# Kernel optimization log

Measured on AMD Instinct MI355X. Metric: run time of the kernel, lower is better.

The kernel has to match this reference:

```python
import jax, jax.numpy as jnp
import numpy as np

N = 100000       # num_nodes
E = 1200000      # num_edges
D = 64           # input feature dim
K = 10           # propagation iterations
ALPHA = 0.1      # teleport probability
H0, H1 = 64, 32  # units_list


def setup_inputs() -> dict:
    key = jax.random.key(0)
    ks = jax.random.split(key, 5)
    x = jax.random.normal(ks[0], (N, D), dtype=jnp.float32)
    edge_index = jax.random.randint(ks[1], (2, E), 0, N, dtype=jnp.int32)
    edge_weight = jax.random.uniform(ks[2], (E,), dtype=jnp.float32)
    # glorot-ish dense params per units_list=[64, 32]
    W0 = jax.random.normal(ks[3], (D, H0), dtype=jnp.float32) * (1.0 / np.sqrt(D))
    b0 = jnp.zeros((H0,), jnp.float32)
    W1 = jax.random.normal(ks[4], (H0, H1), dtype=jnp.float32) * (1.0 / np.sqrt(H0))
    b1 = jnp.zeros((H1,), jnp.float32)
    return dict(x=x, edge_index=edge_index, edge_weight=edge_weight,
                W0=W0, b0=b0, W1=W1, b1=b1)


def reference(x, edge_index, edge_weight, W0, b0, W1, b1):
    n = x.shape[0]
    loop = jnp.arange(n, dtype=edge_index.dtype)
    # GCN renorm: add self-loops with fill weight 1, symmetric D^-1/2 A D^-1/2
    row = jnp.concatenate([edge_index[0], loop])
    col = jnp.concatenate([edge_index[1], loop])
    w = jnp.concatenate([edge_weight, jnp.ones((n,), x.dtype)])
    deg = jax.ops.segment_sum(w, row, num_segments=n)
    dinv = jax.lax.rsqrt(jnp.maximum(deg, 1e-12))
    nw = dinv[row] * w * dinv[col]          # [E+N] normalized edge weights

    # k-hop propagation with running sum: (1/K) sum_k A_hat^k x
    h = x
    acc = jnp.zeros_like(x)
    for _ in range(K):
        h = jax.ops.segment_sum(nw[:, None] * h[row], col, num_segments=n)
        acc = acc + h
    out = acc * ((1.0 - ALPHA) / K) + ALPHA * x

    # dense MLP stack: all but last activated with relu, last linear
    out = jax.nn.relu(out @ W0 + b0)
    out = out @ W1 + b1
    return out
```

## Files before the change

### kernel.cpp

```cpp
#include <hip/hip_runtime.h>
#include <hip/hip_bf16.h>

#define NTHREADS 256
#define GB 1024
#define NB 256
#define BW 512

typedef unsigned int uint32;
typedef unsigned long long u64;


__device__ __forceinline__ float blo(uint32 u) { return __uint_as_float(u << 16); }
__device__ __forceinline__ float bhi(uint32 u) { return __uint_as_float(u & 0xffff0000u); }

__device__ __forceinline__ unsigned short bf16bits(float f) {
    __hip_bfloat16 h = __float2bfloat16(f);
    return *reinterpret_cast<unsigned short*>(&h);
}
__device__ __forceinline__ uint32 pk2(float a, float b) {
    return (uint32)bf16bits(a) | ((uint32)bf16bits(b) << 16);
}


__global__ void deginit_k(float* deg, int n) {
    int i = blockIdx.x * blockDim.x + threadIdx.x;
    if (i < n) deg[i] = 0.f;
}


__global__ __launch_bounds__(256) void histdeg_k(const int* __restrict__ row,
                                                 const int* __restrict__ col,
                                                 const float* __restrict__ w,
                                                 float* deg, int* __restrict__ bh,
                                                 int e, int ch) {
    __shared__ int hist[NB];
    int tid = threadIdx.x;
    hist[tid] = 0;
    __syncthreads();
    int beg = blockIdx.x * ch;
    int end = min(e, beg + ch);
    for (int i = beg + tid; i < end; i += 256) {
        unsafeAtomicAdd(&deg[row[i]], w[i]);
        atomicAdd(&hist[col[i] >> 9], 1);
    }
    __syncthreads();
    bh[(size_t)tid * GB + blockIdx.x] = hist[tid];
}


__global__ __launch_bounds__(256) void scanb_k(int* bh, int* tb) {
    __shared__ int s[256];
    int b = blockIdx.x;
    int tid = threadIdx.x;
    size_t base = (size_t)b * GB + tid * 4;
    int v0 = bh[base], v1 = bh[base + 1], v2 = bh[base + 2], v3 = bh[base + 3];
    int tsum = v0 + v1 + v2 + v3;
    s[tid] = tsum;
    __syncthreads();
    for (int off = 1; off < 256; off <<= 1) {
        int t = (tid >= off) ? s[tid - off] : 0;
        __syncthreads();
        s[tid] += t;
        __syncthreads();
    }
    int excl = s[tid] - tsum;
    bh[base] = excl;
    bh[base + 1] = excl + v0;
    bh[base + 2] = excl + v0 + v1;
    bh[base + 3] = excl + v0 + v1 + v2;
    if (tid == 255) tb[b] = s[255];
}


__global__ void scant_k(const int* __restrict__ tb, int* gb) {
    __shared__ int s[256];
    int tid = threadIdx.x;
    int v = tb[tid];
    s[tid] = v;
    __syncthreads();
    for (int off = 1; off < 256; off <<= 1) {
        int t = (tid >= off) ? s[tid - off] : 0;
        __syncthreads();
        s[tid] += t;
        __syncthreads();
    }
    gb[tid] = s[tid] - v;
    if (tid == 255) gb[256] = s[255];
}


__global__ __launch_bounds__(256) void bscatter_k(const int* __restrict__ row,
                                                  const int* __restrict__ col,
                                                  const float* __restrict__ w,
                                                  const int* __restrict__ bh,
                                                  const int* __restrict__ gb,
                                                  int* __restrict__ st_col,
                                                  u64* __restrict__ st_rw,
                                                  int e, int ch) {
    __shared__ int hist[NB];
    int tid = threadIdx.x;
    hist[tid] = 0;
    __syncthreads();
    int beg = blockIdx.x * ch;
    int end = min(e, beg + ch);
    for (int i = beg + tid; i < end; i += 256) {
        int c = col[i];
        int bk = c >> 9;
        int rank = atomicAdd(&hist[bk], 1);
        int slot = gb[bk] + bh[(size_t)bk * GB + blockIdx.x] + rank;
        st_col[slot] = c;
        st_rw[slot] = (u64)(uint32)row[i] | ((u64)__float_as_uint(w[i]) << 32);
    }
}


__global__ __launch_bounds__(256) void bcount_k(const int* __restrict__ st_col,
                                                const int* __restrict__ gb,
                                                int* __restrict__ counts, int n) {
    __shared__ int cnt[BW];
    int bk = blockIdx.x;
    int tid = threadIdx.x;
    cnt[tid] = 0; cnt[tid + 256] = 0;
    __syncthreads();
    int beg = gb[bk], end = gb[bk + 1];
    for (int j = beg + tid; j < end; j += 256)
        atomicAdd(&cnt[st_col[j] & (BW - 1)], 1);
    __syncthreads();
    int n0 = bk * BW + tid, n1 = n0 + 256;
    if (n0 < n) counts[n0] = cnt[tid];
    if (n1 < n) counts[n1] = cnt[tid + 256];
}


__global__ void scan1_k(const int* __restrict__ counts, int* offsets, int* blockSums, int n) {
    __shared__ int s[256];
    int tid = threadIdx.x;
    int idx = blockIdx.x * 256 + tid;
    int v = (idx < n) ? counts[idx] : 0;
    s[tid] = v;
    __syncthreads();
    for (int off = 1; off < 256; off <<= 1) {
        int t = (tid >= off) ? s[tid - off] : 0;
        __syncthreads();
        s[tid] += t;
        __syncthreads();
    }
    if (idx < n) offsets[idx] = s[tid] - v;
    if (tid == 255) blockSums[blockIdx.x] = s[255];
}

__global__ void scan2_k(int* blockSums, int nb) {
    __shared__ int s[1024];
    int tid = threadIdx.x;
    int v = (tid < nb) ? blockSums[tid] : 0;
    s[tid] = v;
    __syncthreads();
    for (int off = 1; off < 1024; off <<= 1) {
        int t = (tid >= off) ? s[tid - off] : 0;
        __syncthreads();
        s[tid] += t;
        __syncthreads();
    }
    if (tid < nb) blockSums[tid] = s[tid] - v;
}

__global__ void scan3_k(int* offsets, const int* __restrict__ blockSums, int n, int total) {
    int idx = blockIdx.x * blockDim.x + threadIdx.x;
    if (idx < n) offsets[idx] += blockSums[idx >> 8];
    if (idx == n) offsets[n] = total;
}


__global__ __launch_bounds__(256) void bplace_k(const int* __restrict__ st_col,
                                                const u64* __restrict__ st_rw,
                                                const int* __restrict__ gb,
                                                const int* __restrict__ offsets,
                                                u64* __restrict__ csr) {
    __shared__ int cnt[BW];
    int bk = blockIdx.x;
    int tid = threadIdx.x;
    cnt[tid] = 0; cnt[tid + 256] = 0;
    __syncthreads();
    int beg = gb[bk], end = gb[bk + 1];
    for (int j = beg + tid; j < end; j += 256) {
        int c = st_col[j];
        int rank = atomicAdd(&cnt[c & (BW - 1)], 1);
        csr[offsets[c] + rank] = st_rw[j];
    }
}


__global__ void dinv_k(const float* __restrict__ deg, float* dinv, int n) {
    int i = blockIdx.x * blockDim.x + threadIdx.x;
    if (i < n) dinv[i] = rsqrtf(fmaxf(deg[i] + 1.0f, 1e-12f));
}


__global__ void uxseed_k(const float* __restrict__ x, const float* __restrict__ dinv,
                         uint32* __restrict__ ux, int pairs) {
    int i = blockIdx.x * blockDim.x + threadIdx.x;
    if (i < pairs) {
        float di = dinv[i >> 5];
        float2 v = ((const float2*)x)[i];
        ux[i] = pk2(di * v.x, di * v.y);
    }
}


template <int MODE>
__global__ __launch_bounds__(256) void horner4n_k(
    const unsigned short* __restrict__ u_in,
    unsigned short* __restrict__ u_out,
    unsigned short* __restrict__ ybf,
    const unsigned short* __restrict__ ux_bf,
    const float* __restrict__ x,
    const float* __restrict__ dinv,
    const int* __restrict__ offsets,
    const u64* __restrict__ csr,
    int n)
{
    int wv = __builtin_amdgcn_readfirstlane(threadIdx.x >> 6);
    int lane = threadIdx.x & 63;
    int g = lane >> 3;
    int s = lane & 7;
    int nbase = blockIdx.x * 16 + wv * 4;

    int bb[4], ee[4];
#pragma unroll
    for (int m = 0; m < 4; ++m) {
        int node = nbase + m;
        if (node < n) { bb[m] = offsets[node]; ee[m] = offsets[node + 1]; }
        else          { bb[m] = 0; ee[m] = 0; }
    }
    int maxd = max(max(ee[0] - bb[0], ee[1] - bb[1]), max(ee[2] - bb[2], ee[3] - bb[3]));

    float acc[4][8];
#pragma unroll
    for (int m = 0; m < 4; ++m)
#pragma unroll
        for (int i = 0; i < 8; ++i) acc[m][i] = 0.f;

    u64 sw[4];
#pragma unroll
    for (int m = 0; m < 4; ++m) {
        int j = bb[m] + g;
        sw[m] = (j < ee[m]) ? csr[j] : 0ull;
    }

    for (int off = 0; off < maxd; off += 8) {
        uint4 q[4];
#pragma unroll
        for (int m = 0; m < 4; ++m)
            q[m] = ((const uint4*)(u_in + (size_t)(uint32)(sw[m] & 0xffffffffu) * 64))[s];
        u64 swn[4];
#pragma unroll
        for (int m = 0; m < 4; ++m) {
            int j = bb[m] + off + 8 + g;
            swn[m] = (j < ee[m]) ? csr[j] : 0ull;
        }
#pragma unroll
        for (int m = 0; m < 4; ++m) {
            float w = __uint_as_float((uint32)(sw[m] >> 32));
            acc[m][0] = fmaf(w, blo(q[m].x), acc[m][0]);
            acc[m][1] = fmaf(w, bhi(q[m].x), acc[m][1]);
            acc[m][2] = fmaf(w, blo(q[m].y), acc[m][2]);
            acc[m][3] = fmaf(w, bhi(q[m].y), acc[m][3]);
            acc[m][4] = fmaf(w, blo(q[m].z), acc[m][4]);
            acc[m][5] = fmaf(w, bhi(q[m].z), acc[m][5]);
            acc[m][6] = fmaf(w, blo(q[m].w), acc[m][6]);
            acc[m][7] = fmaf(w, bhi(q[m].w), acc[m][7]);
        }
#pragma unroll
        for (int m = 0; m < 4; ++m) sw[m] = swn[m];
    }

#pragma unroll
    for (int mask = 8; mask <= 32; mask <<= 1)
#pragma unroll
        for (int m = 0; m < 4; ++m)
#pragma unroll
            for (int i = 0; i < 8; ++i)
                acc[m][i] += __shfl_xor(acc[m][i], mask);

    float t[8];
#pragma unroll
    for (int i = 0; i < 8; ++i) {
        float a01 = (g == 0) ? acc[0][i] : acc[1][i];
        float a23 = (g == 2) ? acc[2][i] : acc[3][i];
        t[i] = (g < 2) ? a01 : a23;
    }

    if (g < 4) {
        int node = nbase + g;
        if (node < n) {
            float di = dinv[node];
            uint4 zq = ((const uint4*)(u_in + (size_t)node * 64))[s];
            t[0] += blo(zq.x); t[1] += bhi(zq.x);
            t[2] += blo(zq.y); t[3] += bhi(zq.y);
            t[4] += blo(zq.z); t[5] += bhi(zq.z);
            t[6] += blo(zq.w); t[7] += bhi(zq.w);
            if (MODE == 0) {
                float dd = di * di;
                uint4 xq = ((const uint4*)(ux_bf + (size_t)node * 64))[s];
                uint4 o;
                o.x = pk2(fmaf(dd, t[0], blo(xq.x)), fmaf(dd, t[1], bhi(xq.x)));
                o.y = pk2(fmaf(dd, t[2], blo(xq.y)), fmaf(dd, t[3], bhi(xq.y)));
                o.z = pk2(fmaf(dd, t[4], blo(xq.z)), fmaf(dd, t[5], bhi(xq.z)));
                o.w = pk2(fmaf(dd, t[6], blo(xq.w)), fmaf(dd, t[7], bhi(xq.w)));
                ((uint4*)(u_out + (size_t)node * 64))[s] = o;
            } else {
                float c = 0.09f * di;
                const float4* xr = (const float4*)(x + (size_t)node * 64);
                float4 xa = xr[s * 2], xb = xr[s * 2 + 1];
                uint4 o;
                o.x = pk2(fmaf(c, t[0], 0.1f * xa.x), fmaf(c, t[1], 0.1f * xa.y));
                o.y = pk2(fmaf(c, t[2], 0.1f * xa.z), fmaf(c, t[3], 0.1f * xa.w));
                o.z = pk2(fmaf(c, t[4], 0.1f * xb.x), fmaf(c, t[5], 0.1f * xb.y));
                o.w = pk2(fmaf(c, t[6], 0.1f * xb.z), fmaf(c, t[7], 0.1f * xb.w));
                ((uint4*)(ybf + (size_t)node * 64))[s] = o;
            }
        }
    }
}


__global__ __launch_bounds__(256) void mlp_k(const unsigned short* __restrict__ ybf,
                                             const float* __restrict__ W0,
                                             const float* __restrict__ b0,
                                             const float* __restrict__ W1,
                                             const float* __restrict__ b1,
                                             float* __restrict__ out, int n) {
    __shared__ float W0s[64 * 64];
    __shared__ float W1s[64 * 32];
    __shared__ float b0s[64];
    __shared__ float b1s[32];
    __shared__ float z[32][64];
    __shared__ float hid[32][64];
    int tid = threadIdx.x;
    for (int i = tid; i < 64 * 64; i += 256) W0s[i] = W0[i];
    for (int i = tid; i < 64 * 32; i += 256) W1s[i] = W1[i];
    if (tid < 64) b0s[tid] = b0[tid];
    else if (tid < 96) b1s[tid - 64] = b1[tid - 64];

    int base = blockIdx.x * 32;
    const uint32* y32 = (const uint32*)ybf;
    for (int r = 0; r < 4; ++r) {
        int idx = r * 256 + tid;
        int nn = idx >> 5, f2 = idx & 31;
        int node = base + nn;
        uint32 v = (node < n) ? y32[(size_t)node * 32 + f2] : 0u;
        z[nn][f2 * 2]     = blo(v);
        z[nn][f2 * 2 + 1] = bhi(v);
    }
    __syncthreads();
    for (int r = 0; r < 8; ++r) {
        int idx = r * 256 + tid;
        int nn = idx >> 6, j = idx & 63;
        float s = b0s[j];
#pragma unroll
        for (int i = 0; i < 64; ++i) s += z[nn][i] * W0s[i * 64 + j];
        hid[nn][j] = fmaxf(s, 0.f);
    }
    __syncthreads();
    for (int r = 0; r < 4; ++r) {
        int idx = r * 256 + tid;
        int nn = idx >> 5, o = idx & 31;
        int node = base + nn;
        if (node >= n) continue;
        float s = b1s[o];
#pragma unroll
        for (int i = 0; i < 64; ++i) s += hid[nn][i] * W1s[i * 32 + o];
        out[(size_t)node * 32 + o] = s;
    }
}


extern "C" void kernel_launch(void* const* d_in, const int* in_sizes, int n_in,
                              void* d_out, int out_size, void* d_ws, size_t ws_size,
                              hipStream_t stream) {
    const float* x   = (const float*)d_in[0];
    const int*   ei  = (const int*)d_in[1];
    const float* ew  = (const float*)d_in[2];
    const float* W0  = (const float*)d_in[3];
    const float* b0  = (const float*)d_in[4];
    const float* W1  = (const float*)d_in[5];
    const float* b1  = (const float*)d_in[6];
    float* out = (float*)d_out;

    const int N = in_sizes[0] / 64;
    const int E = in_sizes[2];
    const int* row = ei;
    const int* col = ei + E;

    char* p = (char*)d_ws;
    auto alloc = [&](size_t bytes) -> void* {
        void* r = (void*)p;
        p += (bytes + 255) & ~(size_t)255;
        return r;
    };
    float* deg       = (float*)alloc((size_t)N * 4);
    float* dinv      = (float*)alloc((size_t)N * 4);
    int*   bh        = (int*)alloc((size_t)NB * GB * 4);
    int*   tb        = (int*)alloc(NB * 4);
    int*   gb        = (int*)alloc((NB + 1) * 4);
    int*   st_col    = (int*)alloc((size_t)E * 4);
    u64*   st_rw     = (u64*)alloc((size_t)E * 8);
    int*   counts    = (int*)alloc((size_t)N * 4);
    int*   offsets   = (int*)alloc((size_t)(N + 1) * 4);
    int    nb        = (N + 255) / 256;
    int*   blockSums = (int*)alloc((size_t)nb * 4);
    u64*   csr       = (u64*)alloc((size_t)E * 8);
    unsigned short* uxbf = (unsigned short*)alloc((size_t)N * 64 * 2);
    unsigned short* uA   = (unsigned short*)alloc((size_t)N * 64 * 2);
    unsigned short* uB   = (unsigned short*)alloc((size_t)N * 64 * 2);
    unsigned short* ybf  = (unsigned short*)alloc((size_t)N * 64 * 2);

    int gN = (N + NTHREADS - 1) / NTHREADS;
    int ch = (E + GB - 1) / GB;

    deginit_k<<<gN, NTHREADS, 0, stream>>>(deg, N);
    histdeg_k<<<GB, 256, 0, stream>>>(row, col, ew, deg, bh, E, ch);
    scanb_k<<<NB, 256, 0, stream>>>(bh, tb);
    scant_k<<<1, 256, 0, stream>>>(tb, gb);
    bscatter_k<<<GB, 256, 0, stream>>>(row, col, ew, bh, gb, st_col, st_rw, E, ch);
    bcount_k<<<NB, 256, 0, stream>>>(st_col, gb, counts, N);

    scan1_k<<<nb, 256, 0, stream>>>(counts, offsets, blockSums, N);
    scan2_k<<<1, 1024, 0, stream>>>(blockSums, nb);
    scan3_k<<<(N + 1 + NTHREADS - 1) / NTHREADS, NTHREADS, 0, stream>>>(offsets, blockSums, N, E);
    bplace_k<<<NB, 256, 0, stream>>>(st_col, st_rw, gb, offsets, csr);

    dinv_k<<<gN, NTHREADS, 0, stream>>>(deg, dinv, N);
    int pairs = N * 32;
    uxseed_k<<<(pairs + NTHREADS - 1) / NTHREADS, NTHREADS, 0, stream>>>(x, dinv,
                                                                         (uint32*)uxbf, pairs);

    int gP = (N + 15) / 16;
    const unsigned short* ui = uxbf;
    for (int k = 1; k <= 9; ++k) {
        unsigned short* uo = (ui == uA) ? uB : uA;
        horner4n_k<0><<<gP, 256, 0, stream>>>(ui, uo, nullptr, uxbf, x, dinv, offsets, csr, N);
        ui = uo;
    }
    horner4n_k<1><<<gP, 256, 0, stream>>>(ui, nullptr, ybf, uxbf, x, dinv, offsets, csr, N);

    mlp_k<<<(N + 31) / 32, 256, 0, stream>>>(ybf, W0, b0, W1, b1, out, N);
}
```

Before: 508.2 us.

## Compute degrees via row-bucketed sort and run MLP on MFMA bf16

Two separate changes. First, global float atomics on the degree array are replaced by a second bucket sort keyed by row: rows are histogrammed and scattered into the csr buffer, which is reused as scratch, and a per-bucket kernel accumulates degrees in shared memory and writes dinv directly. This removes contended global atomics and the deginit and dinv kernels, at the cost of an extra 8-byte scatter pass over all edges. Second, the MLP uses bf16 MFMA 16x16x32 instructions with swizzled transposed weights in LDS instead of scalar FP32 loops, which lowers precision of the hidden layer and weights to bf16.

After: 428.9 us. 15.6% less time.

```diff
diff --git a/kernel.cpp b/kernel.cpp
--- a/kernel.cpp
+++ b/kernel.cpp
@@ -8,6 +8,8 @@
 
 typedef unsigned int uint32;
 typedef unsigned long long u64;
+typedef __bf16 bf16x8 __attribute__((ext_vector_type(8)));
+typedef float f32x4 __attribute__((ext_vector_type(4)));
 
 
 __device__ __forceinline__ float blo(uint32 u) { return __uint_as_float(u << 16); }
@@ -22,29 +24,23 @@
 }
 
 
-__global__ void deginit_k(float* deg, int n) {
-    int i = blockIdx.x * blockDim.x + threadIdx.x;
-    if (i < n) deg[i] = 0.f;
-}
-
-
-__global__ __launch_bounds__(256) void histdeg_k(const int* __restrict__ row,
-                                                 const int* __restrict__ col,
-                                                 const float* __restrict__ w,
-                                                 float* deg, int* __restrict__ bh,
-                                                 int e, int ch) {
-    __shared__ int hist[NB];
-    int tid = threadIdx.x;
-    hist[tid] = 0;
+__global__ __launch_bounds__(256) void histcols_k(const int* __restrict__ row,
+                                                  const int* __restrict__ col,
+                                                  int* __restrict__ bh, int* __restrict__ bh2,
+                                                  int e, int ch) {
+    __shared__ int h1[NB], h2[NB];
+    int tid = threadIdx.x;
+    h1[tid] = 0; h2[tid] = 0;
     __syncthreads();
     int beg = blockIdx.x * ch;
     int end = min(e, beg + ch);
     for (int i = beg + tid; i < end; i += 256) {
-        unsafeAtomicAdd(&deg[row[i]], w[i]);
-        atomicAdd(&hist[col[i] >> 9], 1);
-    }
-    __syncthreads();
-    bh[(size_t)tid * GB + blockIdx.x] = hist[tid];
+        atomicAdd(&h1[col[i] >> 9], 1);
+        atomicAdd(&h2[row[i] >> 9], 1);
+    }
+    __syncthreads();
+    bh[(size_t)tid * GB + blockIdx.x] = h1[tid];
+    bh2[(size_t)tid * GB + blockIdx.x] = h2[tid];
 }
 
 
@@ -72,7 +68,7 @@
 }
 
 
-__global__ void scant_k(const int* __restrict__ tb, int* gb) {
+__global__ void scant_k(const int* __restrict__ tb, int* gbase) {
     __shared__ int s[256];
     int tid = threadIdx.x;
     int v = tb[tid];
@@ -84,8 +80,8 @@
         s[tid] += t;
         __syncthreads();
     }
-    gb[tid] = s[tid] - v;
-    if (tid == 255) gb[256] = s[255];
+    gbase[tid] = s[tid] - v;
+    if (tid == 255) gbase[256] = s[255];
 }
 
 
@@ -93,24 +89,55 @@
                                                   const int* __restrict__ col,
                                                   const float* __restrict__ w,
                                                   const int* __restrict__ bh,
+                                                  const int* __restrict__ bh2,
                                                   const int* __restrict__ gb,
+                                                  const int* __restrict__ gb2,
                                                   int* __restrict__ st_col,
                                                   u64* __restrict__ st_rw,
+                                                  u64* __restrict__ st2,
                                                   int e, int ch) {
-    __shared__ int hist[NB];
-    int tid = threadIdx.x;
-    hist[tid] = 0;
+    __shared__ int h1[NB], h2[NB];
+    int tid = threadIdx.x;
+    h1[tid] = 0; h2[tid] = 0;
     __syncthreads();
     int beg = blockIdx.x * ch;
     int end = min(e, beg + ch);
     for (int i = beg + tid; i < end; i += 256) {
-        int c = col[i];
+        int c = col[i], r = row[i];
+        float wv = w[i];
+        u64 rec = (u64)(uint32)r | ((u64)__float_as_uint(wv) << 32);
         int bk = c >> 9;
-        int rank = atomicAdd(&hist[bk], 1);
+        int rank = atomicAdd(&h1[bk], 1);
         int slot = gb[bk] + bh[(size_t)bk * GB + blockIdx.x] + rank;
         st_col[slot] = c;
-        st_rw[slot] = (u64)(uint32)row[i] | ((u64)__float_as_uint(w[i]) << 32);
-    }
+        st_rw[slot] = rec;
+        int bk2 = r >> 9;
+        int rank2 = atomicAdd(&h2[bk2], 1);
+        int slot2 = gb2[bk2] + bh2[(size_t)bk2 * GB + blockIdx.x] + rank2;
+        st2[slot2] = rec;
+    }
+}
+
+
+__global__ __launch_bounds__(256) void bdeg_k(const u64* __restrict__ st2,
+                                              const int* __restrict__ gb2,
+                                              float* __restrict__ dinv, int n) {
+    __shared__ float facc[BW];
+    int bk = blockIdx.x;
+    int tid = threadIdx.x;
+    facc[tid] = 0.f; facc[tid + 256] = 0.f;
+    __syncthreads();
+    int beg = gb2[bk], end = gb2[bk + 1];
+    for (int j = beg + tid; j < end; j += 256) {
+        u64 v = st2[j];
+        int r = (int)(uint32)v;
+        float wv = __uint_as_float((uint32)(v >> 32));
+        atomicAdd(&facc[r & (BW - 1)], wv);
+    }
+    __syncthreads();
+    int n0 = bk * BW + tid, n1 = n0 + 256;
+    if (n0 < n) dinv[n0] = rsqrtf(fmaxf(facc[tid] + 1.f, 1e-12f));
+    if (n1 < n) dinv[n1] = rsqrtf(fmaxf(facc[tid + 256] + 1.f, 1e-12f));
 }
 
 
@@ -187,12 +214,6 @@
         int rank = atomicAdd(&cnt[c & (BW - 1)], 1);
         csr[offsets[c] + rank] = st_rw[j];
     }
-}
-
-
-__global__ void dinv_k(const float* __restrict__ deg, float* dinv, int n) {
-    int i = blockIdx.x * blockDim.x + threadIdx.x;
-    if (i < n) dinv[i] = rsqrtf(fmaxf(deg[i] + 1.0f, 1e-12f));
 }
 
 
@@ -324,53 +345,76 @@
 }
 
 
-__global__ __launch_bounds__(256) void mlp_k(const unsigned short* __restrict__ ybf,
-                                             const float* __restrict__ W0,
-                                             const float* __restrict__ b0,
-                                             const float* __restrict__ W1,
-                                             const float* __restrict__ b1,
-                                             float* __restrict__ out, int n) {
-    __shared__ float W0s[64 * 64];
-    __shared__ float W1s[64 * 32];
-    __shared__ float b0s[64];
-    __shared__ float b1s[32];
-    __shared__ float z[32][64];
-    __shared__ float hid[32][64];
-    int tid = threadIdx.x;
-    for (int i = tid; i < 64 * 64; i += 256) W0s[i] = W0[i];
-    for (int i = tid; i < 64 * 32; i += 256) W1s[i] = W1[i];
+__global__ __launch_bounds__(256) void mlp_mfma_k(const unsigned short* __restrict__ ybf,
+                                                  const float* __restrict__ W0,
+                                                  const float* __restrict__ b0,
+                                                  const float* __restrict__ W1,
+                                                  const float* __restrict__ b1,
+                                                  float* __restrict__ out, int n) {
+    __shared__ __align__(16) unsigned short W0t[64 * 64];
+    __shared__ __align__(16) unsigned short W1t[32 * 64];
+    __shared__ __align__(16) unsigned short hidL[4][16 * 64];
+    __shared__ float b0s[64], b1s[32];
+    int tid = threadIdx.x;
+    for (int i = tid; i < 64 * 64; i += 256) {
+        int k = i >> 6, j = i & 63;
+        W0t[j * 64 + (k ^ ((j & 7) << 3))] = bf16bits(W0[i]);
+    }
+    for (int i = tid; i < 64 * 32; i += 256) {
+        int k = i >> 5, j = i & 31;
+        W1t[j * 64 + (k ^ ((j & 7) << 3))] = bf16bits(W1[i]);
+    }
     if (tid < 64) b0s[tid] = b0[tid];
     else if (tid < 96) b1s[tid - 64] = b1[tid - 64];
-
-    int base = blockIdx.x * 32;
-    const uint32* y32 = (const uint32*)ybf;
-    for (int r = 0; r < 4; ++r) {
-        int idx = r * 256 + tid;
-        int nn = idx >> 5, f2 = idx & 31;
-        int node = base + nn;
-        uint32 v = (node < n) ? y32[(size_t)node * 32 + f2] : 0u;
-        z[nn][f2 * 2]     = blo(v);
-        z[nn][f2 * 2 + 1] = bhi(v);
-    }
-    __syncthreads();
-    for (int r = 0; r < 8; ++r) {
-        int idx = r * 256 + tid;
-        int nn = idx >> 6, j = idx & 63;
-        float s = b0s[j];
-#pragma unroll
-        for (int i = 0; i < 64; ++i) s += z[nn][i] * W0s[i * 64 + j];
-        hid[nn][j] = fmaxf(s, 0.f);
-    }
-    __syncthreads();
-    for (int r = 0; r < 4; ++r) {
-        int idx = r * 256 + tid;
-        int nn = idx >> 5, o = idx & 31;
-        int node = base + nn;
-        if (node >= n) continue;
-        float s = b1s[o];
-#pragma unroll
-        for (int i = 0; i < 64; ++i) s += hid[nn][i] * W1s[i * 32 + o];
-        out[(size_t)node * 32 + o] = s;
+    __syncthreads();
+
+    int wave = tid >> 6, lane = tid & 63;
+    int r = lane & 15, g = lane >> 4;
+    int nbase = blockIdx.x * 64 + wave * 16;
+
+    int nodeA = min(nbase + r, n - 1);
+    const bf16x8* yrow = (const bf16x8*)(ybf + (size_t)nodeA * 64);
+    bf16x8 A0 = yrow[g];
+    bf16x8 A1 = yrow[4 + g];
+
+#pragma unroll
+    for (int t = 0; t < 4; ++t) {
+        int j = t * 16 + r;
+        int sj = j & 7;
+        const bf16x8* wcol = (const bf16x8*)(W0t + j * 64);
+        bf16x8 B0 = wcol[g ^ sj];
+        bf16x8 B1 = wcol[(4 + g) ^ sj];
+        float bv = b0s[j];
+        f32x4 acc = {bv, bv, bv, bv};
+        acc = __builtin_amdgcn_mfma_f32_16x16x32_bf16(A0, B0, acc, 0, 0, 0);
+        acc = __builtin_amdgcn_mfma_f32_16x16x32_bf16(A1, B1, acc, 0, 0, 0);
+#pragma unroll
+        for (int v = 0; v < 4; ++v) {
+            int i = g * 4 + v;
+            hidL[wave][i * 64 + (j ^ ((i & 7) << 3))] = bf16bits(fmaxf(acc[v], 0.f));
+        }
+    }
+
+    const bf16x8* hrow = (const bf16x8*)(hidL[wave] + r * 64);
+    int sr = r & 7;
+    bf16x8 HA0 = hrow[g ^ sr];
+    bf16x8 HA1 = hrow[(4 + g) ^ sr];
+#pragma unroll
+    for (int t = 0; t < 2; ++t) {
+        int j = t * 16 + r;
+        int sj = j & 7;
+        const bf16x8* wcol = (const bf16x8*)(W1t + j * 64);
+        bf16x8 B0 = wcol[g ^ sj];
+        bf16x8 B1 = wcol[(4 + g) ^ sj];
+        float bv = b1s[j];
+        f32x4 acc = {bv, bv, bv, bv};
+        acc = __builtin_amdgcn_mfma_f32_16x16x32_bf16(HA0, B0, acc, 0, 0, 0);
+        acc = __builtin_amdgcn_mfma_f32_16x16x32_bf16(HA1, B1, acc, 0, 0, 0);
+#pragma unroll
+        for (int v = 0; v < 4; ++v) {
+            int node = nbase + g * 4 + v;
+            if (node < n) out[(size_t)node * 32 + j] = acc[v];
+        }
     }
 }
 
@@ -398,11 +442,13 @@
         p += (bytes + 255) & ~(size_t)255;
         return r;
     };
-    float* deg       = (float*)alloc((size_t)N * 4);
     float* dinv      = (float*)alloc((size_t)N * 4);
     int*   bh        = (int*)alloc((size_t)NB * GB * 4);
+    int*   bh2       = (int*)alloc((size_t)NB * GB * 4);
     int*   tb        = (int*)alloc(NB * 4);
+    int*   tb2       = (int*)alloc(NB * 4);
     int*   gb        = (int*)alloc((NB + 1) * 4);
+    int*   gb2       = (int*)alloc((NB + 1) * 4);
     int*   st_col    = (int*)alloc((size_t)E * 4);
     u64*   st_rw     = (u64*)alloc((size_t)E * 8);
     int*   counts    = (int*)alloc((size_t)N * 4);
@@ -415,14 +461,16 @@
     unsigned short* uB   = (unsigned short*)alloc((size_t)N * 64 * 2);
     unsigned short* ybf  = (unsigned short*)alloc((size_t)N * 64 * 2);
 
-    int gN = (N + NTHREADS - 1) / NTHREADS;
     int ch = (E + GB - 1) / GB;
 
-    deginit_k<<<gN, NTHREADS, 0, stream>>>(deg, N);
-    histdeg_k<<<GB, 256, 0, stream>>>(row, col, ew, deg, bh, E, ch);
+    histcols_k<<<GB, 256, 0, stream>>>(row, col, bh, bh2, E, ch);
     scanb_k<<<NB, 256, 0, stream>>>(bh, tb);
+    scanb_k<<<NB, 256, 0, stream>>>(bh2, tb2);
     scant_k<<<1, 256, 0, stream>>>(tb, gb);
-    bscatter_k<<<GB, 256, 0, stream>>>(row, col, ew, bh, gb, st_col, st_rw, E, ch);
+    scant_k<<<1, 256, 0, stream>>>(tb2, gb2);
+    bscatter_k<<<GB, 256, 0, stream>>>(row, col, ew, bh, bh2, gb, gb2,
+                                       st_col, st_rw, csr , E, ch);
+    bdeg_k<<<NB, 256, 0, stream>>>(csr , gb2, dinv, N);
     bcount_k<<<NB, 256, 0, stream>>>(st_col, gb, counts, N);
 
     scan1_k<<<nb, 256, 0, stream>>>(counts, offsets, blockSums, N);
@@ -430,7 +478,6 @@
     scan3_k<<<(N + 1 + NTHREADS - 1) / NTHREADS, NTHREADS, 0, stream>>>(offsets, blockSums, N, E);
     bplace_k<<<NB, 256, 0, stream>>>(st_col, st_rw, gb, offsets, csr);
 
-    dinv_k<<<gN, NTHREADS, 0, stream>>>(deg, dinv, N);
     int pairs = N * 32;
     uxseed_k<<<(pairs + NTHREADS - 1) / NTHREADS, NTHREADS, 0, stream>>>(x, dinv,
                                                                          (uint32*)uxbf, pairs);
@@ -444,5 +491,5 @@
     }
     horner4n_k<1><<<gP, 256, 0, stream>>>(ui, nullptr, ybf, uxbf, x, dinv, offsets, csr, N);
 
-    mlp_k<<<(N + 31) / 32, 256, 0, stream>>>(ybf, W0, b0, W1, b1, out, N);
-}
+    mlp_mfma_k<<<(N + 63) / 64, 256, 0, stream>>>(ybf, W0, b0, W1, b1, out, N);
+}
```
